# Kernel tuning notes

Measured on AMD Instinct MI355X. Metric: run time of the kernel, lower is better.

## Reference

```python
import jax, jax.numpy as jnp
import numpy as np

N_BINS = 15
N = 4194304
C = 64

def setup_inputs() -> dict:
    key = jax.random.key(0)
    k1, k2 = jax.random.split(key)
    logits = jax.random.normal(k1, (N, C), dtype=jnp.float32) * 2.0
    softmaxes = jax.nn.softmax(logits, axis=-1)
    labels = jax.random.randint(k2, (N,), 0, C, dtype=jnp.int64)
    return {"softmaxes": softmaxes, "labels": labels}

def reference(softmaxes, labels):
    n = softmaxes.shape[0]
    confidences = jnp.max(softmaxes, axis=1)            # [N]
    predictions = jnp.argmax(softmaxes, axis=1)         # [N]
    accuracies = (predictions == labels).astype(jnp.float32)

    # bin i covers (i/n_bins, (i+1)/n_bins]; conf == 0 falls in no bin (matches torch gt/le)
    bounds = jnp.linspace(0.0, 1.0, N_BINS + 1)
    bid = jnp.searchsorted(bounds, confidences, side="left") - 1   # [N]
    valid = (bid >= 0) & (bid < N_BINS)
    seg = jnp.where(valid, bid, N_BINS)                 # dump invalid into extra segment

    ones = jnp.ones_like(confidences)
    counts = jax.ops.segment_sum(ones, seg, num_segments=N_BINS + 1)[:N_BINS]
    conf_sum = jax.ops.segment_sum(confidences, seg, num_segments=N_BINS + 1)[:N_BINS]
    acc_sum = jax.ops.segment_sum(accuracies, seg, num_segments=N_BINS + 1)[:N_BINS]

    denom = jnp.maximum(counts, 1.0)
    avg_conf = conf_sum / denom
    avg_acc = acc_sum / denom
    prop = counts / jnp.float32(n)
    gaps = jnp.where(counts > 0, jnp.abs(avg_conf - avg_acc) * prop, 0.0)
    return jnp.sum(gaps).reshape(1)
```

## Files before the change

### kernel.cpp

```cpp
#include <hip/hip_runtime.h>

#define N_BINS 15
#define NREP 8
#define NSPREAD 32
#define SEG (3 * N_BINS)
#define HWORDS (NREP * SEG)

__device__ __forceinline__ unsigned umax_(unsigned a, unsigned b) { return a > b ? a : b; }

#define OFFBITS 0x3C800000u

__device__ __forceinline__ unsigned row_key(const float4 v, const int sub) {
    const int base = sub << 2;
    unsigned k0 = ((umax_(__float_as_uint(v.x), OFFBITS) - OFFBITS) << 6) | (unsigned)(63 - base);
    unsigned k1 = ((umax_(__float_as_uint(v.y), OFFBITS) - OFFBITS) << 6) | (unsigned)(62 - base);
    unsigned k2 = ((umax_(__float_as_uint(v.z), OFFBITS) - OFFBITS) << 6) | (unsigned)(61 - base);
    unsigned k3 = ((umax_(__float_as_uint(v.w), OFFBITS) - OFFBITS) << 6) | (unsigned)(60 - base);
    return umax_(umax_(k0, k1), umax_(k2, k3));
}

__device__ __forceinline__ void commit(float* hrep, unsigned key, int sub, int lab) {
    if (sub < 3) {
        const float m = __uint_as_float((key >> 6) + OFFBITS);
        int bid = 0;
        #pragma unroll
        for (int j = 1; j <= N_BINS; ++j)
            bid += ((float)j / 15.0f < m) ? 1 : 0;
        if (bid > N_BINS - 1) bid = N_BINS - 1;
        float val;
        if (sub == 0)      val = 1.0f;
        else if (sub == 1) val = m;
        else {
            const int pred = 63 - (int)(key & 63u);
            val = (pred == lab) ? 1.0f : 0.0f;
        }
        atomicAdd(&hrep[sub * N_BINS + bid], val);
    }
}

__global__ __launch_bounds__(256) void ece_partial_kernel(
    const float* __restrict__ sm, const int* __restrict__ labels,
    float* __restrict__ g, int n)
{
    __shared__ float s_hist[HWORDS];
    const int tid = threadIdx.x;
    for (int i = tid; i < HWORDS; i += 256) s_hist[i] = 0.f;
    __syncthreads();

    const int sub = tid & 15;
    float* hrep = s_hist + ((tid >> 4) & (NREP - 1)) * SEG;
    const long long step = (long long)gridDim.x * 16;
    long long row = (long long)blockIdx.x * 16 + (tid >> 4);

    for (; row + step < n; row += 2 * step) {
        const float4 v0 = *reinterpret_cast<const float4*>(sm + (row << 6) + (sub << 2));
        const float4 v1 = *reinterpret_cast<const float4*>(sm + ((row + step) << 6) + (sub << 2));
        int lab0 = 0, lab1 = 0;
        if (sub == 2) { lab0 = labels[row]; lab1 = labels[row + step]; }

        unsigned key0 = row_key(v0, sub);
        unsigned key1 = row_key(v1, sub);
        #pragma unroll
        for (int off = 1; off < 16; off <<= 1) {
            key0 = umax_(key0, (unsigned)__shfl_xor((int)key0, off));
            key1 = umax_(key1, (unsigned)__shfl_xor((int)key1, off));
        }
        commit(hrep, key0, sub, lab0);
        commit(hrep, key1, sub, lab1);
    }
    if (row < n) {
        const float4 v0 = *reinterpret_cast<const float4*>(sm + (row << 6) + (sub << 2));
        int lab0 = 0;
        if (sub == 2) lab0 = labels[row];
        unsigned key0 = row_key(v0, sub);
        #pragma unroll
        for (int off = 1; off < 16; off <<= 1)
            key0 = umax_(key0, (unsigned)__shfl_xor((int)key0, off));
        commit(hrep, key0, sub, lab0);
    }

    __syncthreads();
    if (tid < SEG) {
        float v = 0.f;
        #pragma unroll
        for (int r = 0; r < NREP; ++r) v += s_hist[r * SEG + tid];
        atomicAdd(&g[(blockIdx.x & (NSPREAD - 1)) * SEG + tid], v);
    }
}

__global__ void ece_final_kernel(const float* __restrict__ g, float* __restrict__ out, int n)
{
    __shared__ float s[SEG];
    const int tid = threadIdx.x;
    if (tid < SEG) {
        float v = 0.f;
        #pragma unroll
        for (int r = 0; r < NSPREAD; ++r) v += g[r * SEG + tid];
        s[tid] = v;
    }
    __syncthreads();
    if (tid == 0) {
        float total = 0.f;
        #pragma unroll
        for (int i = 0; i < N_BINS; ++i) {
            const float c = s[i];
            if (c > 0.f) {
                const float d = fmaxf(c, 1.f);
                total += fabsf(s[N_BINS + i] / d - s[2*N_BINS + i] / d) * (c / (float)n);
            }
        }
        out[0] = total;
    }
}

extern "C" void kernel_launch(void* const* d_in, const int* in_sizes, int n_in,
                              void* d_out, int out_size, void* d_ws, size_t ws_size,
                              hipStream_t stream) {
    const float* sm     = (const float*)d_in[0];
    const int*   labels = (const int*)d_in[1];
    float* out = (float*)d_out;
    float* g   = (float*)d_ws;
    const int n = in_sizes[1];

    hipMemsetAsync(g, 0, NSPREAD * SEG * sizeof(float), stream);

    const int grid = 2048;
    ece_partial_kernel<<<grid, 256, 0, stream>>>(sm, labels, g, n);
    ece_final_kernel<<<1, 64, 0, stream>>>(g, out, n);
}
```

Baseline: 219.2 us.

## Process four contiguous rows per 16-lane group and spread histogram commits across lanes

```diff
diff --git a/kernel.cpp b/kernel.cpp
--- a/kernel.cpp
+++ b/kernel.cpp
@@ -19,14 +19,18 @@
     return umax_(umax_(k0, k1), umax_(k2, k3));
 }
 
-__device__ __forceinline__ void commit(float* hrep, unsigned key, int sub, int lab) {
+__device__ __forceinline__ int bin_of(float conf) {
+    int bid = 0;
+    #pragma unroll
+    for (int j = 1; j <= N_BINS; ++j)
+        bid += ((float)j / 15.0f < conf) ? 1 : 0;
+    return bid > N_BINS - 1 ? N_BINS - 1 : bid;
+}
+
+__device__ __forceinline__ void commit1(float* hrep, unsigned key, int sub, int lab) {
     if (sub < 3) {
         const float m = __uint_as_float((key >> 6) + OFFBITS);
-        int bid = 0;
-        #pragma unroll
-        for (int j = 1; j <= N_BINS; ++j)
-            bid += ((float)j / 15.0f < m) ? 1 : 0;
-        if (bid > N_BINS - 1) bid = N_BINS - 1;
+        const int bid = bin_of(m);
         float val;
         if (sub == 0)      val = 1.0f;
         else if (sub == 1) val = m;
@@ -48,35 +52,62 @@
     __syncthreads();
 
     const int sub = tid & 15;
-    float* hrep = s_hist + ((tid >> 4) & (NREP - 1)) * SEG;
-    const long long step = (long long)gridDim.x * 16;
-    long long row = (long long)blockIdx.x * 16 + (tid >> 4);
+    const int grp = tid >> 4;
+    float* hrep = s_hist + (grp & (NREP - 1)) * SEG;
+    const int col = sub << 2;
 
-    for (; row + step < n; row += 2 * step) {
-        const float4 v0 = *reinterpret_cast<const float4*>(sm + (row << 6) + (sub << 2));
-        const float4 v1 = *reinterpret_cast<const float4*>(sm + ((row + step) << 6) + (sub << 2));
-        int lab0 = 0, lab1 = 0;
-        if (sub == 2) { lab0 = labels[row]; lab1 = labels[row + step]; }
+    const long long R = (long long)gridDim.x * 64;
+    const long long nfull = ((long long)n / R) * R;
 
-        unsigned key0 = row_key(v0, sub);
-        unsigned key1 = row_key(v1, sub);
+    for (long long rb = (long long)blockIdx.x * 64 + ((long long)grp << 2);
+         rb < nfull; rb += R)
+    {
+        const float4 v0 = *reinterpret_cast<const float4*>(sm + (rb << 6) + col);
+        const float4 v1 = *reinterpret_cast<const float4*>(sm + ((rb + 1) << 6) + col);
+        const float4 v2 = *reinterpret_cast<const float4*>(sm + ((rb + 2) << 6) + col);
+        const float4 v3 = *reinterpret_cast<const float4*>(sm + ((rb + 3) << 6) + col);
+        int lab = 0;
+        if ((unsigned)(sub - 8) < 4u) lab = labels[rb + (sub & 3)];
+
+        unsigned k0 = row_key(v0, sub);
+        unsigned k1 = row_key(v1, sub);
+        unsigned k2 = row_key(v2, sub);
+        unsigned k3 = row_key(v3, sub);
         #pragma unroll
         for (int off = 1; off < 16; off <<= 1) {
-            key0 = umax_(key0, (unsigned)__shfl_xor((int)key0, off));
-            key1 = umax_(key1, (unsigned)__shfl_xor((int)key1, off));
+            k0 = umax_(k0, (unsigned)__shfl_xor((int)k0, off));
+            k1 = umax_(k1, (unsigned)__shfl_xor((int)k1, off));
+            k2 = umax_(k2, (unsigned)__shfl_xor((int)k2, off));
+            k3 = umax_(k3, (unsigned)__shfl_xor((int)k3, off));
         }
-        commit(hrep, key0, sub, lab0);
-        commit(hrep, key1, sub, lab1);
+
+        if (sub < 12) {
+            const int r = sub & 3;
+            const int m = sub >> 2;
+            unsigned key = (r == 0) ? k0 : (r == 1) ? k1 : (r == 2) ? k2 : k3;
+            const float conf = __uint_as_float((key >> 6) + OFFBITS);
+            const int bid = bin_of(conf);
+            float val;
+            if (m == 0)      val = 1.0f;
+            else if (m == 1) val = conf;
+            else {
+                const int pred = 63 - (int)(key & 63u);
+                val = (pred == lab) ? 1.0f : 0.0f;
+            }
+            atomicAdd(&hrep[m * N_BINS + bid], val);
+        }
     }
-    if (row < n) {
-        const float4 v0 = *reinterpret_cast<const float4*>(sm + (row << 6) + (sub << 2));
-        int lab0 = 0;
-        if (sub == 2) lab0 = labels[row];
-        unsigned key0 = row_key(v0, sub);
+
+    for (long long row = nfull + (long long)blockIdx.x * 16 + grp;
+         row < n; row += (long long)gridDim.x * 16)
+    {
+        const float4 v = *reinterpret_cast<const float4*>(sm + (row << 6) + col);
+        int lab = (sub == 2) ? labels[row] : 0;
+        unsigned key = row_key(v, sub);
         #pragma unroll
         for (int off = 1; off < 16; off <<= 1)
-            key0 = umax_(key0, (unsigned)__shfl_xor((int)key0, off));
-        commit(hrep, key0, sub, lab0);
+            key = umax_(key, (unsigned)__shfl_xor((int)key, off));
+        commit1(hrep, key, sub, lab);
     }
 
     __syncthreads();
```

Result: faster. 199.2 us (-9.1%).
